# Kernel tuning notes

Measured on AMD Instinct MI355X. Metric: run time of the kernel, lower is better.

## Reference

```python
import jax, jax.numpy as jnp
import numpy as np
import math

T = 32
DIM = 1024
BATCH = 4096
ETA = 1.0


def setup_inputs() -> dict:
    key = jax.random.key(0)
    k1, k2, k3, k4 = jax.random.split(key, 4)
    x = jax.random.normal(k1, (BATCH, DIM), dtype=jnp.float32)
    mu = jax.random.uniform(k2, (T, DIM), dtype=jnp.float32, minval=-0.5, maxval=0.5)
    rho = jax.random.uniform(k3, (T, DIM), dtype=jnp.float32, minval=-0.5, maxval=0.5)
    # stochastic Beta(gamma_1, gamma_2) draws in the original (scipy beta.rvs);
    # passed as an explicit input, kept strictly inside (0, 1)
    beta_samples = jax.random.uniform(k4, (BATCH, T), dtype=jnp.float32,
                                      minval=0.01, maxval=0.99)
    return {"x": x, "mu": mu, "rho": rho, "beta_samples": beta_samples}


def _forward(x, mu, rho, beta_samples):
    B, D = x.shape
    Tn = mu.shape[0]
    log2pi = math.log(2.0 * math.pi)

    std = jnp.log1p(jnp.exp(rho))              # [T, D]
    log_std_sum = jnp.sum(jnp.log(std), axis=-1)   # [T]
    inv_var = 1.0 / (std * std)                # [T, D]

    # Diagonal Gaussian log-prob, batched over all T components via GEMMs
    quad = (jnp.einsum('bd,td->bt', x * x, inv_var)
            - 2.0 * jnp.einsum('bd,td->bt', x, mu * inv_var)
            + jnp.sum(mu * mu * inv_var, axis=-1)[None, :])   # [B, T]
    log_pdfs = -0.5 * D * log2pi - log_std_sum[None, :] - 0.5 * quad  # [B, T]

    # entropy of each diagonal Gaussian, broadcast to batch
    entropy = (D / 2.0) * (log2pi + 1.0) + log_std_sum   # [T]
    entropy = jnp.broadcast_to(entropy[None, :], (B, Tn))

    # stick-breaking weights: pi = mix_weights(beta)[:, :-1]
    beta1m_cumprod = jnp.cumprod(1.0 - beta_samples, axis=-1)   # [B, T]
    pi = beta_samples * jnp.concatenate(
        [jnp.ones((B, 1), x.dtype), beta1m_cumprod[:, :-1]], axis=-1)  # [B, T]
    log_pi = jnp.log(pi)

    # get_phi
    kl_gaussian = log_pdfs + entropy            # [B, T]
    N_t_gaussian = jnp.sum(kl_gaussian, axis=0, keepdims=True)  # [1, T]
    N_t_pi = jnp.sum(log_pi, axis=0, keepdims=True)             # [1, T]
    mix = N_t_pi / (N_t_gaussian + N_t_pi)      # [1, T]
    kl = mix * kl_gaussian + (1.0 - mix) * log_pi
    phi_new = jax.nn.softmax(kl, axis=1)        # [B, T]
    kl_g_mixed = mix * kl_gaussian              # [B, T]

    likelihood = jnp.mean(jnp.sum(phi_new * kl_g_mixed, axis=1), axis=0)  # scalar
    return likelihood


def reference(x, mu, rho, beta_samples):
    return _forward(x, mu, rho, beta_samples)
```

## Files before the change

### kernel.cpp

```cpp
#include <hip/hip_runtime.h>
#include <math.h>

constexpr int NT = 32;
constexpr int ND = 1024;
constexpr int NB = 4096;
constexpr int NBLK_MAIN = 512;

typedef float f2 __attribute__((ext_vector_type(2)));

constexpr int OFF_M2C = 32768;
constexpr int OFF_C2  = 65536;
constexpr int OFF_KLG = 65600;
constexpr int OFF_LPI = 196672;
constexpr int OFF_PG  = 327744;
constexpr int OFF_PP  = 344128;

__global__ __launch_bounds__(256) void k_stats(const float* __restrict__ mu,
                                               const float* __restrict__ rho,
                                               float* __restrict__ ws,
                                               float* __restrict__ out) {
  float* ivc = ws;
  float* m2c = ws + OFF_M2C;
  float* c2  = ws + OFF_C2;

  const int t = blockIdx.x;
  const int c = threadIdx.x;

  float4 mu4  = reinterpret_cast<const float4*>(mu  + t * ND)[c];
  float4 rho4 = reinterpret_cast<const float4*>(rho + t * ND)[c];

  float rr[4] = {rho4.x, rho4.y, rho4.z, rho4.w};
  float mm[4] = {mu4.x,  mu4.y,  mu4.z,  mu4.w};
  float iv[4], m2[4];
  float c2p = 0.0f;
#pragma unroll
  for (int j = 0; j < 4; ++j) {
    float sd  = log1pf(expf(rr[j]));
    float ivv = 1.0f / (sd * sd);
    iv[j] = ivv;
    m2[j] = -2.0f * mm[j] * ivv;
    c2p  += mm[j] * mm[j] * ivv;
  }
  float4 iv4 = {iv[0], iv[1], iv[2], iv[3]};
  float4 m24 = {m2[0], m2[1], m2[2], m2[3]};
  reinterpret_cast<float4*>(ivc)[c * NT + t] = iv4;
  reinterpret_cast<float4*>(m2c)[c * NT + t] = m24;

#pragma unroll
  for (int m = 32; m >= 1; m >>= 1) c2p += __shfl_xor(c2p, m, 64);
  __shared__ float red[4];
  const int wave = threadIdx.x >> 6, lane = threadIdx.x & 63;
  if (lane == 0) red[wave] = c2p;
  __syncthreads();
  if (threadIdx.x == 0) {
    c2[t] = red[0] + red[1] + red[2] + red[3];
    if (t == 0) out[0] = 0.0f;
  }
}

__global__ __launch_bounds__(512, 4) void k_main(const float* __restrict__ x,
                                                 const float* __restrict__ beta,
                                                 float* __restrict__ ws) {
  const float* ivc = ws;
  const float* m2c = ws + OFF_M2C;
  const float* c2  = ws + OFF_C2;
  float* klg = ws + OFF_KLG;
  float* lpi = ws + OFF_LPI;
  float* Pg  = ws + OFF_PG;
  float* Pp  = ws + OFF_PP;

  const int tid  = threadIdx.x;
  const int q    = tid >> 6;
  const int lane = tid & 63;
  const int h = lane >> 5, t = lane & 31;
  const int row0 = blockIdx.x * 8;

  __shared__ float4 xs4[8 * 256];
  __shared__ float part[8][8][32];

  {
    const float4* xg4 = reinterpret_cast<const float4*>(x) + (size_t)row0 * 256;
#pragma unroll
    for (int k = 0; k < 4; ++k) {
      xs4[k * 512 + tid] = xg4[k * 512 + tid];
    }
  }
  __syncthreads();

  const int c0 = q * 32 + h * 16;
  const float4* ivp = reinterpret_cast<const float4*>(ivc) + (size_t)c0 * NT + t;
  const float4* m2p = reinterpret_cast<const float4*>(m2c) + (size_t)c0 * NT + t;
  const float4* xsp = xs4 + c0;

  f2 a2[8];
#pragma unroll
  for (int r = 0; r < 8; ++r) a2[r] = (f2){0.f, 0.f};

#pragma unroll 4
  for (int i = 0; i < 16; ++i) {
    float4 iv4 = ivp[(size_t)i * NT];
    float4 m24 = m2p[(size_t)i * NT];
    const f2 ivl = {iv4.x, iv4.y}, ivh = {iv4.z, iv4.w};
    const f2 ml  = {m24.x, m24.y}, mh  = {m24.z, m24.w};
#pragma unroll
    for (int r = 0; r < 8; ++r) {
      float4 xv = xsp[r * 256 + i];
      const f2 xl = {xv.x, xv.y}, xh = {xv.z, xv.w};
      a2[r] = __builtin_elementwise_fma(xl, __builtin_elementwise_fma(xl, ivl, ml), a2[r]);
      a2[r] = __builtin_elementwise_fma(xh, __builtin_elementwise_fma(xh, ivh, mh), a2[r]);
    }
  }
#pragma unroll
  for (int r = 0; r < 8; ++r) {
    float s = a2[r].x + a2[r].y;
    s += __shfl_xor(s, 32, 64);
    if (h == 0) part[q][r][t] = s;
  }
  __syncthreads();

  const int rr = tid >> 5, t2 = tid & 31;
  float kv = 0.f, lp = 0.f;
  if (tid < 256) {
    float quad = 0.f;
#pragma unroll
    for (int qq = 0; qq < 8; ++qq) quad += part[qq][rr][t2];
    kv = 512.0f - 0.5f * (quad + c2[t2]);
    klg[(size_t)(row0 + rr) * NT + t2] = kv;

    const float b = beta[(size_t)(row0 + rr) * NT + t2];
    const float l1m = log1pf(-b);
    float s = l1m;
#pragma unroll
    for (int d = 1; d < 32; d <<= 1) {
      float v = __shfl_up(s, (unsigned)d, 32);
      if (t2 >= d) s += v;
    }
    lp = logf(b) + (s - l1m);
    lpi[(size_t)(row0 + rr) * NT + t2] = lp;
  }
  __syncthreads();
  if (tid < 256) {
    part[0][rr][t2] = kv;
    part[1][rr][t2] = lp;
  }
  __syncthreads();
  if (tid < 32) {
    float sg = 0.f, sp = 0.f;
#pragma unroll
    for (int r = 0; r < 8; ++r) { sg += part[0][r][tid]; sp += part[1][r][tid]; }
    Pg[(size_t)blockIdx.x * NT + tid] = sg;
    Pp[(size_t)blockIdx.x * NT + tid] = sp;
  }
}

__global__ __launch_bounds__(512) void k_final(const float* __restrict__ ws,
                                               float* __restrict__ out) {
  const float* klg = ws + OFF_KLG;
  const float* lpi = ws + OFF_LPI;
  const float* Pg  = ws + OFF_PG;
  const float* Pp  = ws + OFF_PP;

  const int tid  = threadIdx.x;
  const int wave = tid >> 6, lane = tid & 63;
  const int t = tid & 31;
  const int g = tid >> 5;

  __shared__ float ngF[32], npF[32];
  __shared__ float redG[8][32], redP[8][32];
  __shared__ float red[8];

  {
    float sg = 0.f, sp = 0.f;
#pragma unroll 8
    for (int b = g; b < NBLK_MAIN; b += 16) {
      sg += Pg[(size_t)b * NT + t];
      sp += Pp[(size_t)b * NT + t];
    }
    sg += __shfl_xor(sg, 32, 64);
    sp += __shfl_xor(sp, 32, 64);
    if (lane < 32) { redG[wave][t] = sg; redP[wave][t] = sp; }
  }
  __syncthreads();
  if (tid < 32) {
    float ng = 0.f, np = 0.f;
#pragma unroll
    for (int w = 0; w < 8; ++w) { ng += redG[w][tid]; np += redP[w][tid]; }
    ngF[tid] = ng;
    npF[tid] = np;
  }
  __syncthreads();

  const int row = blockIdx.x * 16 + g;
  const float kg = klg[(size_t)row * NT + t];
  const float lp = lpi[(size_t)row * NT + t];
  const float ng = ngF[t], np = npF[t];
  const float mix  = np / (ng + np);
  const float klgm = mix * kg;
  const float kl   = klgm + (1.0f - mix) * lp;

  float m = kl;
#pragma unroll
  for (int mk = 16; mk >= 1; mk >>= 1) m = fmaxf(m, __shfl_xor(m, mk, 64));
  const float e = expf(kl - m);
  float num = e * klgm, den = e;
#pragma unroll
  for (int mk = 16; mk >= 1; mk >>= 1) {
    num += __shfl_xor(num, mk, 64);
    den += __shfl_xor(den, mk, 64);
  }
  float s = num / den;
  s += __shfl_xor(s, 32, 64);

  if (lane == 0) red[wave] = s;
  __syncthreads();
  if (tid == 0) {
    float tot = 0.f;
#pragma unroll
    for (int w = 0; w < 8; ++w) tot += red[w];
    atomicAdd(out, tot * (1.0f / (float)NB));
  }
}

extern "C" void kernel_launch(void* const* d_in, const int* in_sizes, int n_in,
                              void* d_out, int out_size, void* d_ws, size_t ws_size,
                              hipStream_t stream) {
  const float* x    = (const float*)d_in[0];
  const float* mu   = (const float*)d_in[1];
  const float* rho  = (const float*)d_in[2];
  const float* beta = (const float*)d_in[3];
  float* out = (float*)d_out;
  float* ws  = (float*)d_ws;

  hipLaunchKernelGGL(k_stats, dim3(32),        dim3(256), 0, stream, mu, rho, ws, out);
  hipLaunchKernelGGL(k_main,  dim3(NBLK_MAIN), dim3(512), 0, stream, x, beta, ws);
  hipLaunchKernelGGL(k_final, dim3(256),       dim3(512), 0, stream, ws, out);
}
```

Before: 30.56 us.

## Compute quadratic term with bf16x3 split MFMA instead of FP32 FMA

Replaces the scalar FP32 FMA accumulation of x^2*inv_var - 2x*mu*inv_var with MFMA 16x16x32 bf16 instructions. It uses a hi/lo bf16 split (three products per pair) to keep roughly FP32 accuracy. The interleaved [x^2, x] and [inv_var, -2mu*inv_var] operands fold both GEMMs into one K=2048 contraction. Blocks now cover 16 rows (256 blocks), and x is converted to bf16 pairs in shared memory over four K stages. This trades the FP32 VALU cost for conversion overhead and possible precision loss, and B is read straight from global memory without reuse staging.

```diff
diff --git a/kernel.cpp b/kernel.cpp
--- a/kernel.cpp
+++ b/kernel.cpp
@@ -4,47 +4,59 @@
 constexpr int NT = 32;
 constexpr int ND = 1024;
 constexpr int NB = 4096;
-constexpr int NBLK_MAIN = 512;
-
-typedef float f2 __attribute__((ext_vector_type(2)));
-
-constexpr int OFF_M2C = 32768;
+constexpr int NBLK_MAIN = 256;
+
+typedef short bf16x8 __attribute__((ext_vector_type(8)));
+typedef float f32x4  __attribute__((ext_vector_type(4)));
+
 constexpr int OFF_C2  = 65536;
 constexpr int OFF_KLG = 65600;
 constexpr int OFF_LPI = 196672;
 constexpr int OFF_PG  = 327744;
-constexpr int OFF_PP  = 344128;
+constexpr int OFF_PP  = 335936;
+
+__device__ __forceinline__ unsigned short bf16h(float x) {
+  unsigned u = __float_as_uint(x);
+  u = u + 0x7FFFu + ((u >> 16) & 1u);
+  return (unsigned short)(u >> 16);
+}
+__device__ __forceinline__ float bf16f(unsigned short h) {
+  return __uint_as_float(((unsigned)h) << 16);
+}
 
 __global__ __launch_bounds__(256) void k_stats(const float* __restrict__ mu,
                                                const float* __restrict__ rho,
                                                float* __restrict__ ws,
                                                float* __restrict__ out) {
-  float* ivc = ws;
-  float* m2c = ws + OFF_M2C;
-  float* c2  = ws + OFF_C2;
+  unsigned short* Bh = reinterpret_cast<unsigned short*>(ws);
+  unsigned short* Bl = Bh + 65536;
+  float* c2 = ws + OFF_C2;
 
   const int t = blockIdx.x;
   const int c = threadIdx.x;
 
-  float4 mu4  = reinterpret_cast<const float4*>(mu  + t * ND)[c];
-  float4 rho4 = reinterpret_cast<const float4*>(rho + t * ND)[c];
-
-  float rr[4] = {rho4.x, rho4.y, rho4.z, rho4.w};
-  float mm[4] = {mu4.x,  mu4.y,  mu4.z,  mu4.w};
-  float iv[4], m2[4];
+  float4 mu4 = reinterpret_cast<const float4*>(mu  + t * ND)[c];
+  float4 rh4 = reinterpret_cast<const float4*>(rho + t * ND)[c];
+  float mm[4] = {mu4.x, mu4.y, mu4.z, mu4.w};
+  float rr[4] = {rh4.x, rh4.y, rh4.z, rh4.w};
+
+  bf16x8 hv, lv;
   float c2p = 0.0f;
 #pragma unroll
   for (int j = 0; j < 4; ++j) {
     float sd  = log1pf(expf(rr[j]));
     float ivv = 1.0f / (sd * sd);
-    iv[j] = ivv;
-    m2[j] = -2.0f * mm[j] * ivv;
-    c2p  += mm[j] * mm[j] * ivv;
-  }
-  float4 iv4 = {iv[0], iv[1], iv[2], iv[3]};
-  float4 m24 = {m2[0], m2[1], m2[2], m2[3]};
-  reinterpret_cast<float4*>(ivc)[c * NT + t] = iv4;
-  reinterpret_cast<float4*>(m2c)[c * NT + t] = m24;
+    float m2v = -2.0f * mm[j] * ivv;
+    c2p += mm[j] * mm[j] * ivv;
+    unsigned short ih = bf16h(ivv);
+    unsigned short il = bf16h(ivv - bf16f(ih));
+    unsigned short mh = bf16h(m2v);
+    unsigned short ml = bf16h(m2v - bf16f(mh));
+    hv[2 * j] = (short)ih; hv[2 * j + 1] = (short)mh;
+    lv[2 * j] = (short)il; lv[2 * j + 1] = (short)ml;
+  }
+  *reinterpret_cast<bf16x8*>(Bh + (size_t)t * 2048 + c * 8) = hv;
+  *reinterpret_cast<bf16x8*>(Bl + (size_t)t * 2048 + c * 8) = lv;
 
 #pragma unroll
   for (int m = 32; m >= 1; m >>= 1) c2p += __shfl_xor(c2p, m, 64);
@@ -58,96 +70,123 @@
   }
 }
 
-__global__ __launch_bounds__(512, 4) void k_main(const float* __restrict__ x,
-                                                 const float* __restrict__ beta,
-                                                 float* __restrict__ ws) {
-  const float* ivc = ws;
-  const float* m2c = ws + OFF_M2C;
-  const float* c2  = ws + OFF_C2;
+__global__ __launch_bounds__(512) void k_main(const float* __restrict__ x,
+                                              const float* __restrict__ beta,
+                                              float* __restrict__ ws) {
+  const unsigned short* Bh = reinterpret_cast<const unsigned short*>(ws);
+  const unsigned short* Bl = Bh + 65536;
+  const float* c2 = ws + OFF_C2;
   float* klg = ws + OFF_KLG;
   float* lpi = ws + OFF_LPI;
   float* Pg  = ws + OFF_PG;
   float* Pp  = ws + OFF_PP;
 
   const int tid  = threadIdx.x;
-  const int q    = tid >> 6;
+  const int w    = tid >> 6;
   const int lane = tid & 63;
-  const int h = lane >> 5, t = lane & 31;
-  const int row0 = blockIdx.x * 8;
-
-  __shared__ float4 xs4[8 * 256];
-  __shared__ float part[8][8][32];
+  const int l15  = lane & 15;
+  const int g4   = lane >> 4;
+  const int row0 = blockIdx.x * 16;
+
+  __shared__ __align__(16) short Ah[16 * 520];
+  __shared__ __align__(16) short Al[16 * 520];
+  __shared__ float part[8][16][32];
+
+  const int srow = tid >> 5;
+  const int dch  = tid & 31;
+  const float4* xr4 =
+      reinterpret_cast<const float4*>(x + (size_t)(row0 + srow) * ND) + dch * 2;
+
+  float4 xa = xr4[0], xb = xr4[1];
+
+  f32x4 acc0 = {0.f, 0.f, 0.f, 0.f};
+  f32x4 acc1 = {0.f, 0.f, 0.f, 0.f};
+
+#pragma unroll
+  for (int s = 0; s < 4; ++s) {
+    __syncthreads();
+    {
+      float xv[8] = {xa.x, xa.y, xa.z, xa.w, xb.x, xb.y, xb.z, xb.w};
+      bf16x8 h0, h1, lo0, lo1;
+#pragma unroll
+      for (int j = 0; j < 8; ++j) {
+        float sq = xv[j] * xv[j];
+        unsigned short sh = bf16h(sq);
+        unsigned short sl = bf16h(sq - bf16f(sh));
+        unsigned short xh = bf16h(xv[j]);
+        unsigned short xl = bf16h(xv[j] - bf16f(xh));
+        if (j < 4) {
+          h0[2 * j] = (short)sh;  h0[2 * j + 1] = (short)xh;
+          lo0[2 * j] = (short)sl; lo0[2 * j + 1] = (short)xl;
+        } else {
+          h1[2 * (j - 4)] = (short)sh;  h1[2 * (j - 4) + 1] = (short)xh;
+          lo1[2 * (j - 4)] = (short)sl; lo1[2 * (j - 4) + 1] = (short)xl;
+        }
+      }
+      const int ab = srow * 520 + dch * 16;
+      *reinterpret_cast<bf16x8*>(&Ah[ab])     = h0;
+      *reinterpret_cast<bf16x8*>(&Ah[ab + 8]) = h1;
+      *reinterpret_cast<bf16x8*>(&Al[ab])     = lo0;
+      *reinterpret_cast<bf16x8*>(&Al[ab + 8]) = lo1;
+    }
+    if (s < 3) { xa = xr4[(s + 1) * 64]; xb = xr4[(s + 1) * 64 + 1]; }
+    __syncthreads();
+
+#pragma unroll
+    for (int st = 0; st < 2; ++st) {
+      const int kl = w * 64 + st * 32 + g4 * 8;
+      const int kg = s * 512 + kl;
+      bf16x8 afh = *reinterpret_cast<const bf16x8*>(&Ah[l15 * 520 + kl]);
+      bf16x8 afl = *reinterpret_cast<const bf16x8*>(&Al[l15 * 520 + kl]);
+      bf16x8 bh0 = *reinterpret_cast<const bf16x8*>(Bh + (size_t)l15 * 2048 + kg);
+      bf16x8 bh1 = *reinterpret_cast<const bf16x8*>(Bh + (size_t)(16 + l15) * 2048 + kg);
+      bf16x8 bl0 = *reinterpret_cast<const bf16x8*>(Bl + (size_t)l15 * 2048 + kg);
+      bf16x8 bl1 = *reinterpret_cast<const bf16x8*>(Bl + (size_t)(16 + l15) * 2048 + kg);
+      acc0 = __builtin_amdgcn_mfma_f32_16x16x32_bf16(afh, bh0, acc0, 0, 0, 0);
+      acc1 = __builtin_amdgcn_mfma_f32_16x16x32_bf16(afh, bh1, acc1, 0, 0, 0);
+      acc0 = __builtin_amdgcn_mfma_f32_16x16x32_bf16(afh, bl0, acc0, 0, 0, 0);
+      acc1 = __builtin_amdgcn_mfma_f32_16x16x32_bf16(afh, bl1, acc1, 0, 0, 0);
+      acc0 = __builtin_amdgcn_mfma_f32_16x16x32_bf16(afl, bh0, acc0, 0, 0, 0);
+      acc1 = __builtin_amdgcn_mfma_f32_16x16x32_bf16(afl, bh1, acc1, 0, 0, 0);
+    }
+  }
 
   {
-    const float4* xg4 = reinterpret_cast<const float4*>(x) + (size_t)row0 * 256;
-#pragma unroll
-    for (int k = 0; k < 4; ++k) {
-      xs4[k * 512 + tid] = xg4[k * 512 + tid];
-    }
-  }
-  __syncthreads();
-
-  const int c0 = q * 32 + h * 16;
-  const float4* ivp = reinterpret_cast<const float4*>(ivc) + (size_t)c0 * NT + t;
-  const float4* m2p = reinterpret_cast<const float4*>(m2c) + (size_t)c0 * NT + t;
-  const float4* xsp = xs4 + c0;
-
-  f2 a2[8];
-#pragma unroll
-  for (int r = 0; r < 8; ++r) a2[r] = (f2){0.f, 0.f};
-
-#pragma unroll 4
-  for (int i = 0; i < 16; ++i) {
-    float4 iv4 = ivp[(size_t)i * NT];
-    float4 m24 = m2p[(size_t)i * NT];
-    const f2 ivl = {iv4.x, iv4.y}, ivh = {iv4.z, iv4.w};
-    const f2 ml  = {m24.x, m24.y}, mh  = {m24.z, m24.w};
-#pragma unroll
-    for (int r = 0; r < 8; ++r) {
-      float4 xv = xsp[r * 256 + i];
-      const f2 xl = {xv.x, xv.y}, xh = {xv.z, xv.w};
-      a2[r] = __builtin_elementwise_fma(xl, __builtin_elementwise_fma(xl, ivl, ml), a2[r]);
-      a2[r] = __builtin_elementwise_fma(xh, __builtin_elementwise_fma(xh, ivh, mh), a2[r]);
-    }
-  }
-#pragma unroll
-  for (int r = 0; r < 8; ++r) {
-    float s = a2[r].x + a2[r].y;
-    s += __shfl_xor(s, 32, 64);
-    if (h == 0) part[q][r][t] = s;
+    const int crow = g4 * 4;
+#pragma unroll
+    for (int v = 0; v < 4; ++v) {
+      part[w][crow + v][l15]      = acc0[v];
+      part[w][crow + v][16 + l15] = acc1[v];
+    }
   }
   __syncthreads();
 
   const int rr = tid >> 5, t2 = tid & 31;
-  float kv = 0.f, lp = 0.f;
-  if (tid < 256) {
-    float quad = 0.f;
-#pragma unroll
-    for (int qq = 0; qq < 8; ++qq) quad += part[qq][rr][t2];
-    kv = 512.0f - 0.5f * (quad + c2[t2]);
-    klg[(size_t)(row0 + rr) * NT + t2] = kv;
-
-    const float b = beta[(size_t)(row0 + rr) * NT + t2];
-    const float l1m = log1pf(-b);
-    float s = l1m;
-#pragma unroll
-    for (int d = 1; d < 32; d <<= 1) {
-      float v = __shfl_up(s, (unsigned)d, 32);
-      if (t2 >= d) s += v;
-    }
-    lp = logf(b) + (s - l1m);
-    lpi[(size_t)(row0 + rr) * NT + t2] = lp;
-  }
-  __syncthreads();
-  if (tid < 256) {
-    part[0][rr][t2] = kv;
-    part[1][rr][t2] = lp;
-  }
+  float quad = 0.f;
+#pragma unroll
+  for (int ww = 0; ww < 8; ++ww) quad += part[ww][rr][t2];
+  const float kv = 512.0f - 0.5f * (quad + c2[t2]);
+  klg[(size_t)(row0 + rr) * NT + t2] = kv;
+
+  const float b = beta[(size_t)(row0 + rr) * NT + t2];
+  const float l1m = log1pf(-b);
+  float sc = l1m;
+#pragma unroll
+  for (int d = 1; d < 32; d <<= 1) {
+    float v = __shfl_up(sc, (unsigned)d, 32);
+    if (t2 >= d) sc += v;
+  }
+  const float lp = logf(b) + (sc - l1m);
+  lpi[(size_t)(row0 + rr) * NT + t2] = lp;
+
+  __syncthreads();
+  part[0][rr][t2] = kv;
+  part[1][rr][t2] = lp;
   __syncthreads();
   if (tid < 32) {
     float sg = 0.f, sp = 0.f;
 #pragma unroll
-    for (int r = 0; r < 8; ++r) { sg += part[0][r][tid]; sp += part[1][r][tid]; }
+    for (int r = 0; r < 16; ++r) { sg += part[0][r][tid]; sp += part[1][r][tid]; }
     Pg[(size_t)blockIdx.x * NT + tid] = sg;
     Pp[(size_t)blockIdx.x * NT + tid] = sp;
   }
@@ -171,7 +210,7 @@
 
   {
     float sg = 0.f, sp = 0.f;
-#pragma unroll 8
+#pragma unroll 4
     for (int b = g; b < NBLK_MAIN; b += 16) {
       sg += Pg[(size_t)b * NT + t];
       sp += Pp[(size_t)b * NT + t];
```

Result: no change. 30.17 us (-1.3%).
